# Optimization experiments

Measured on AMD Instinct MI355X. Metric: run time of the kernel, lower is better.

## Reference

```python
import jax, jax.numpy as jnp
import numpy as np

EPS = 1e-4

def _ema(unit_embeddings, unit_confidence, unit_mask):
    # unit_embeddings: (B, J, D), unit_confidence/unit_mask: (B, J)
    emb_j = jnp.swapaxes(unit_embeddings, 0, 1)        # (J, B, D)
    p_j = jnp.swapaxes(unit_confidence, 0, 1)          # (J, B)
    m_j = jnp.swapaxes(unit_mask, 0, 1)                # (J, B)

    B, _, D = unit_embeddings.shape
    prev0 = jnp.zeros((B, D), dtype=unit_embeddings.dtype)

    def step(prev, inp):
        emb, p, m = inp                                # (B,D), (B,), (B,)
        p = jnp.clip(p, EPS, 1.0 - EPS)[:, None]       # (B,1)
        m = m[:, None]                                 # (B,1)
        cur = jnp.where(m, emb, jnp.zeros_like(emb))
        new = jnp.where(m, p * cur + (1.0 - p) * prev, prev)
        return new, new

    _, smoothed = jax.lax.scan(step, prev0, (emb_j, p_j, m_j))  # (J, B, D)
    return jnp.swapaxes(smoothed, 0, 1)                # (B, J, D)

def _upsample(smoothed, boundary_mask):
    # smoothed: (B, J, D), boundary_mask: (B, L) bool
    J = smoothed.shape[1]
    idx = jnp.cumsum(boundary_mask.astype(jnp.int32), axis=1) - 1
    idx = jnp.clip(idx, 0, J - 1)                      # (B, L)
    return jnp.take_along_axis(smoothed, idx[:, :, None], axis=1)  # (B, L, D)

def setup_inputs() -> dict:
    key = jax.random.key(0)
    k1, k2, k3, k4 = jax.random.split(key, 4)
    B, J, L, D = 16, 1024, 4096, 512
    unit_embeddings = jax.random.normal(k1, (B, J, D), dtype=jnp.float32)
    unit_confidence = jax.random.uniform(k2, (B, J), dtype=jnp.float32)
    unit_mask = jax.random.randint(k3, (B, J), 0, 2).astype(bool)
    boundary_mask = jax.random.randint(k4, (B, L), 0, 2).astype(bool)
    return {
        "unit_embeddings": unit_embeddings,
        "unit_confidence": unit_confidence,
        "unit_mask": unit_mask,
        "boundary_mask": boundary_mask,
    }

def reference(unit_embeddings, unit_confidence, unit_mask, boundary_mask):
    smoothed = _ema(unit_embeddings, unit_confidence, unit_mask)
    frames = _upsample(smoothed, boundary_mask)
    return frames
```

## Files before the change

### kernel.cpp

```cpp
#include <hip/hip_runtime.h>
#include <cstddef>

namespace {
constexpr int Bn = 16;
constexpr int Jn = 1024;
constexpr int Ln = 4096;
constexpr int Dn = 512;
constexpr int G  = 32;
constexpr int C  = Jn / G;
constexpr float kEps = 1e-4f;
constexpr int PASS1_BLOCKS = Bn * C;
}

__device__ __forceinline__ unsigned short bf16rne(float x) {
  unsigned u = __float_as_uint(x);
  unsigned r = (u + 0x7fffu + ((u >> 16) & 1u)) >> 16;
  return (unsigned short)r;
}
__device__ __forceinline__ float bf16tof(unsigned short h) {
  return __uint_as_float(((unsigned)h) << 16);
}

__global__ __launch_bounds__(128) void k_fused1(
    const float* __restrict__ emb, const float* __restrict__ conf,
    const int* __restrict__ mask, const int* __restrict__ bnd,
    unsigned short* __restrict__ localh, float* __restrict__ E,
    float* __restrict__ PA, float* __restrict__ Ap, int* __restrict__ idx) {
  int blk = blockIdx.x;
  int t = threadIdx.x;
  if (blk < PASS1_BLOCKS) {
    int b = blk / C, c = blk % C;
    int base = b * Jn + c * G;
    float4 s = make_float4(0.f, 0.f, 0.f, 0.f);
    float prod = 1.0f;
#pragma unroll 8
    for (int i = 0; i < G; ++i) {
      int j = base + i;
      float p = conf[j];
      p = fminf(fmaxf(p, kEps), 1.0f - kEps);
      bool m = (mask[j] != 0);
      float q = 1.0f - p;
      float4 e = ((const float4*)(emb + (size_t)j * Dn))[t];
      if (m) {
        s.x = p * e.x + q * s.x;
        s.y = p * e.y + q * s.y;
        s.z = p * e.z + q * s.z;
        s.w = p * e.w + q * s.w;
        prod *= q;
      }
      ushort4 h;
      h.x = bf16rne(s.x); h.y = bf16rne(s.y);
      h.z = bf16rne(s.z); h.w = bf16rne(s.w);
      ((ushort4*)(localh + (size_t)j * Dn))[t] = h;
      if (t == 0) PA[j] = prod;
    }
    ((float4*)(E + (size_t)blk * Dn))[t] = s;
    if (t == 0) Ap[blk] = prod;
  } else {
    int b = blk - PASS1_BLOCKS;
    const int per = Ln / 128;
    const int* row = bnd + (size_t)b * Ln;
    int s = 0;
#pragma unroll 8
    for (int i = 0; i < per; ++i) s += (row[t * per + i] != 0) ? 1 : 0;

    __shared__ int sh[128];
    sh[t] = s;
    __syncthreads();
    for (int off = 1; off < 128; off <<= 1) {
      int v = (t >= off) ? sh[t - off] : 0;
      __syncthreads();
      sh[t] += v;
      __syncthreads();
    }
    int run = sh[t] - s;
#pragma unroll 8
    for (int i = 0; i < per; ++i) {
      run += (row[t * per + i] != 0) ? 1 : 0;
      int v = run - 1;
      v = v < 0 ? 0 : (v > Jn - 1 ? Jn - 1 : v);
      idx[(size_t)b * Ln + t * per + i] = v;
    }
  }
}

__global__ __launch_bounds__(64) void k_chunk_start(
    const float* __restrict__ E, const float* __restrict__ Ap,
    float* __restrict__ S) {
  int tg = blockIdx.x * 64 + threadIdx.x;
  int b = tg / (Dn / 4), d4 = tg % (Dn / 4);
  float4 s = make_float4(0.f, 0.f, 0.f, 0.f);
#pragma unroll 8
  for (int c = 0; c < C; ++c) {
    ((float4*)(S + ((size_t)(b * C + c)) * Dn))[d4] = s;
    float a = Ap[b * C + c];
    float4 e = ((const float4*)(E + ((size_t)(b * C + c)) * Dn))[d4];
    s.x = e.x + a * s.x;
    s.y = e.y + a * s.y;
    s.z = e.z + a * s.z;
    s.w = e.w + a * s.w;
  }
}

__global__ __launch_bounds__(256) void k_gather(
    const unsigned short* __restrict__ localh, const float* __restrict__ PA,
    const float* __restrict__ S, const int* __restrict__ idx,
    float* __restrict__ out) {
  unsigned bid = blockIdx.x;
  unsigned sb = (bid & 7u) * 4096u + (bid >> 3);
  size_t tid = (size_t)sb * 256 + threadIdx.x;
  int d4 = (int)(tid & (Dn / 4 - 1));
  size_t bl = tid >> 7;
  int j = idx[bl];
  size_t b = bl >> 12;
  int c = j >> 5;
  float pa = PA[b * Jn + (size_t)j];
  float4 sc = ((const float4*)(S + (b * C + (size_t)c) * Dn))[d4];
  ushort4 lh = ((const ushort4*)(localh + (b * Jn + (size_t)j) * Dn))[d4];
  float4 o;
  o.x = bf16tof(lh.x) + pa * sc.x;
  o.y = bf16tof(lh.y) + pa * sc.y;
  o.z = bf16tof(lh.z) + pa * sc.z;
  o.w = bf16tof(lh.w) + pa * sc.w;
  ((float4*)out)[tid] = o;
}

extern "C" void kernel_launch(void* const* d_in, const int* in_sizes, int n_in,
                              void* d_out, int out_size, void* d_ws, size_t ws_size,
                              hipStream_t stream) {
  const float* emb  = (const float*)d_in[0];
  const float* conf = (const float*)d_in[1];
  const int*   mask = (const int*)d_in[2];
  const int*   bnd  = (const int*)d_in[3];
  float* out = (float*)d_out;

  float* ws = (float*)d_ws;
  unsigned short* localh = (unsigned short*)ws;
  float* E   = ws + (size_t)Bn * Jn * Dn / 2;
  float* S   = E + (size_t)Bn * C * Dn;
  float* PA  = S + (size_t)Bn * C * Dn;
  float* Ap  = PA + (size_t)Bn * Jn;
  int*   idx = (int*)(Ap + Bn * C);

  hipLaunchKernelGGL(k_fused1, dim3(PASS1_BLOCKS + Bn), dim3(128), 0, stream,
                     emb, conf, mask, bnd, localh, E, PA, Ap, idx);
  hipLaunchKernelGGL(k_chunk_start, dim3(Bn * (Dn / 4) / 64), dim3(64), 0, stream,
                     E, Ap, S);
  size_t total4 = (size_t)Bn * Ln * (Dn / 4);
  hipLaunchKernelGGL(k_gather, dim3((unsigned)(total4 / 256)), dim3(256), 0, stream,
                     localh, PA, S, idx, out);
}
```

Baseline: 176.8 us.

## Halve EMA chunk size, remap pass-1 blocks per XCD, use nontemporal loads/stores

The chunk length drops from 32 to 16, doubling the number of pass-1 blocks and halving each block's serial recurrence length, while the chunk-start scan gets twice as many sequential steps. Pass-1 blocks are remapped so each XCD handles two batches, which is meant to keep a batch's localh/PA data in one L2 and improve gather locality. Embedding reads and the large output writes use nontemporal hints to avoid polluting cache. Arithmetic is rewritten with ext_vector_type, which is cosmetic.

```diff
diff --git a/kernel.cpp b/kernel.cpp
--- a/kernel.cpp
+++ b/kernel.cpp
@@ -6,11 +6,13 @@
 constexpr int Jn = 1024;
 constexpr int Ln = 4096;
 constexpr int Dn = 512;
-constexpr int G  = 32;
+constexpr int G  = 16;
 constexpr int C  = Jn / G;
 constexpr float kEps = 1e-4f;
 constexpr int PASS1_BLOCKS = Bn * C;
 }
+
+typedef float fvec4 __attribute__((ext_vector_type(4)));
 
 __device__ __forceinline__ unsigned short bf16rne(float x) {
   unsigned u = __float_as_uint(x);
@@ -29,9 +31,12 @@
   int blk = blockIdx.x;
   int t = threadIdx.x;
   if (blk < PASS1_BLOCKS) {
-    int b = blk / C, c = blk % C;
+    int xcd  = blk & 7;
+    int slot = blk >> 3;
+    int b = 2 * xcd + (slot & 1);
+    int c = slot >> 1;
     int base = b * Jn + c * G;
-    float4 s = make_float4(0.f, 0.f, 0.f, 0.f);
+    fvec4 s = (fvec4)(0.f);
     float prod = 1.0f;
 #pragma unroll 8
     for (int i = 0; i < G; ++i) {
@@ -40,12 +45,9 @@
       p = fminf(fmaxf(p, kEps), 1.0f - kEps);
       bool m = (mask[j] != 0);
       float q = 1.0f - p;
-      float4 e = ((const float4*)(emb + (size_t)j * Dn))[t];
+      fvec4 e = __builtin_nontemporal_load(((const fvec4*)(emb + (size_t)j * Dn)) + t);
       if (m) {
-        s.x = p * e.x + q * s.x;
-        s.y = p * e.y + q * s.y;
-        s.z = p * e.z + q * s.z;
-        s.w = p * e.w + q * s.w;
+        s = p * e + q * s;
         prod *= q;
       }
       ushort4 h;
@@ -54,8 +56,8 @@
       ((ushort4*)(localh + (size_t)j * Dn))[t] = h;
       if (t == 0) PA[j] = prod;
     }
-    ((float4*)(E + (size_t)blk * Dn))[t] = s;
-    if (t == 0) Ap[blk] = prod;
+    ((fvec4*)(E + ((size_t)(b * C + c)) * Dn))[t] = s;
+    if (t == 0) Ap[b * C + c] = prod;
   } else {
     int b = blk - PASS1_BLOCKS;
     const int per = Ln / 128;
@@ -89,16 +91,13 @@
     float* __restrict__ S) {
   int tg = blockIdx.x * 64 + threadIdx.x;
   int b = tg / (Dn / 4), d4 = tg % (Dn / 4);
-  float4 s = make_float4(0.f, 0.f, 0.f, 0.f);
+  fvec4 s = (fvec4)(0.f);
 #pragma unroll 8
   for (int c = 0; c < C; ++c) {
-    ((float4*)(S + ((size_t)(b * C + c)) * Dn))[d4] = s;
+    ((fvec4*)(S + ((size_t)(b * C + c)) * Dn))[d4] = s;
     float a = Ap[b * C + c];
-    float4 e = ((const float4*)(E + ((size_t)(b * C + c)) * Dn))[d4];
-    s.x = e.x + a * s.x;
-    s.y = e.y + a * s.y;
-    s.z = e.z + a * s.z;
-    s.w = e.w + a * s.w;
+    fvec4 e = ((const fvec4*)(E + ((size_t)(b * C + c)) * Dn))[d4];
+    s = e + a * s;
   }
 }
 
@@ -113,16 +112,16 @@
   size_t bl = tid >> 7;
   int j = idx[bl];
   size_t b = bl >> 12;
-  int c = j >> 5;
+  int c = j >> 4;
   float pa = PA[b * Jn + (size_t)j];
-  float4 sc = ((const float4*)(S + (b * C + (size_t)c) * Dn))[d4];
+  fvec4 sc = ((const fvec4*)(S + (b * C + (size_t)c) * Dn))[d4];
   ushort4 lh = ((const ushort4*)(localh + (b * Jn + (size_t)j) * Dn))[d4];
-  float4 o;
+  fvec4 o;
   o.x = bf16tof(lh.x) + pa * sc.x;
   o.y = bf16tof(lh.y) + pa * sc.y;
   o.z = bf16tof(lh.z) + pa * sc.z;
   o.w = bf16tof(lh.w) + pa * sc.w;
-  ((float4*)out)[tid] = o;
+  __builtin_nontemporal_store(o, ((fvec4*)out) + tid);
 }
 
 extern "C" void kernel_launch(void* const* d_in, const int* in_sizes, int n_in,
```

New measurement: 174.1 us. No clear change (-1.6%).
